# Kernel tuning notes

Hardware: AMD Instinct MI355X
Metric: run time of the kernel (lower is better)

## Reference

```python
import jax, jax.numpy as jnp
import numpy as np

B, T = 2, 512
D, H, DFF = 1024, 16, 4096
V, CSL = 32000, 16
NL, NDL = 4, 2
MAXLEN = 1024
DH = D // H


def generate_ar_mask(L, csl):
    m = np.zeros((2 * L, 2 * L), dtype=bool)
    for i in range(L):
        m[:i] = True
        m[L + (i // csl) * csl: L + i] = True
    return jnp.asarray(m)


def generate_block_ntp_mask(L, csl):
    m = np.zeros((2 * L, 2 * L), dtype=bool)
    for c in range(L // csl):
        if c - 1 >= 0:
            m[:(c - 1) * csl] = True
        m[L + c * csl: L + (c + 1) * csl] = True
    return jnp.asarray(m)


def layernorm(x, g, b, eps=1e-5):
    mu = x.mean(-1, keepdims=True)
    var = x.var(-1, keepdims=True)
    return (x - mu) / jnp.sqrt(var + eps) * g + b


def block(x, mask, p):
    ln1g, ln1b, wqkv, bqkv, wo, bo, ln2g, ln2b, w1, b1, w2, b2 = p
    h = layernorm(x, ln1g, ln1b)
    qkv = h @ wqkv + bqkv                       # [B,S,3D]
    q, k, v = jnp.split(qkv, 3, axis=-1)
    bs, S, _ = x.shape
    q = q.reshape(bs, S, H, DH).transpose(0, 2, 1, 3)
    k = k.reshape(bs, S, H, DH).transpose(0, 2, 1, 3)
    v = v.reshape(bs, S, H, DH).transpose(0, 2, 1, 3)
    scores = jnp.einsum('bhqd,bhkd->bhqk', q, k) / jnp.sqrt(jnp.asarray(DH, x.dtype))
    scores = jnp.where(mask, scores, jnp.asarray(-1e9, x.dtype))
    attn = jax.nn.softmax(scores, axis=-1)
    o = jnp.einsum('bhqk,bhkd->bhqd', attn, v)
    o = o.transpose(0, 2, 1, 3).reshape(bs, S, D)
    x = x + (o @ wo + bo)
    h = layernorm(x, ln2g, ln2b)
    return x + (jax.nn.gelu(h @ w1 + b1, approximate=False) @ w2 + b2)


def setup_inputs():
    key = jax.random.key(0)
    ks = jax.random.split(key, 6)

    def pstack(k, n):
        kk = jax.random.split(k, 4)
        return dict(
            ln1g=jnp.ones((n, D)), ln1b=jnp.zeros((n, D)),
            wqkv=0.02 * jax.random.normal(kk[0], (n, D, 3 * D)), bqkv=jnp.zeros((n, 3 * D)),
            wo=0.02 * jax.random.normal(kk[1], (n, D, D)), bo=jnp.zeros((n, D)),
            ln2g=jnp.ones((n, D)), ln2b=jnp.zeros((n, D)),
            w1=0.02 * jax.random.normal(kk[2], (n, D, DFF)), b1=jnp.zeros((n, DFF)),
            w2=0.02 * jax.random.normal(kk[3], (n, DFF, D)), b2=jnp.zeros((n, D)))

    body = pstack(ks[0], NL)
    dec = pstack(ks[1], NDL)
    inp = {
        'tok_ids': jax.random.randint(ks[2], (B, T), 0, V),
        'tok_emb': 0.02 * jax.random.normal(ks[3], (V, D)),
        'pos_emb': 0.02 * jax.random.normal(ks[4], (MAXLEN, D)),
        'mask_tokens': 0.02 * jax.random.normal(ks[5], (1, CSL, D)),
    }
    for kname, vv in body.items():
        inp['b_' + kname] = vv
    for kname, vv in dec.items():
        inp['d_' + kname] = vv
    return inp


def reference(tok_ids, tok_emb, pos_emb, mask_tokens,
              b_ln1g, b_ln1b, b_wqkv, b_bqkv, b_wo, b_bo, b_ln2g, b_ln2b, b_w1, b_b1, b_w2, b_b2,
              d_ln1g, d_ln1b, d_wqkv, d_bqkv, d_wo, d_bo, d_ln2g, d_ln2b, d_w1, d_b1, d_w2, d_b2):
    Bq, Tq = tok_ids.shape
    pos = jnp.tile(jnp.arange(Tq), 2)            # pos ids repeated for both halves
    emb_pos = pos_emb[pos]                       # [2T, D], broadcast over batch
    mask_ids = jnp.tile(mask_tokens, (Bq, Tq // CSL, 1))
    x = jnp.concatenate([tok_emb[tok_ids], mask_ids], axis=1) + emb_pos[None]

    body_mask = generate_block_ntp_mask(Tq, CSL)
    bp = (b_ln1g, b_ln1b, b_wqkv, b_bqkv, b_wo, b_bo, b_ln2g, b_ln2b, b_w1, b_b1, b_w2, b_b2)
    for i in range(NL):
        x = block(x, body_mask, tuple(p[i] for p in bp))

    ar_mask = generate_ar_mask(Tq, CSL)
    dp = (d_ln1g, d_ln1b, d_wqkv, d_bqkv, d_wo, d_bo, d_ln2g, d_ln2b, d_w1, d_b1, d_w2, d_b2)
    for i in range(NDL):
        x = block(x, ar_mask, tuple(p[i] for p in dp))

    logits = (x @ tok_emb.T)[:, Tq + 1:, :]      # [B, T-1, V]
    tgt = tok_ids[:, :-1].reshape(-1)
    logits = logits.reshape(-1, V)
    logp = jax.nn.log_softmax(logits, axis=-1)
    loss = -jnp.take_along_axis(logp, tgt[:, None], axis=1).mean()
    return loss
```

## Files before the change

kernel.cpp:

```cpp
#include <hip/hip_runtime.h>
#include <hip/hip_bf16.h>
#include <math.h>

#define DD   1024
#define HHN  16
#define DHD  64
#define DFFN 4096
#define VV   32000
#define BBN  2
#define TTN  512
#define SSN  1024
#define NRN  2048

typedef __attribute__((ext_vector_type(8))) short short8;
typedef __attribute__((ext_vector_type(4))) float f32x4;

enum : long {
    LSTR    = 12582912,
    OFF_QKV = 0,
    OFF_WO  = 3145728,
    OFF_W1  = 4194304,
    OFF_W2  = 8388608
};

struct P24 { const float* p[24]; };

__device__ __forceinline__ unsigned short f2bf(float f) {
    __hip_bfloat16 h = __float2bfloat16(f);
    return __builtin_bit_cast(unsigned short, h);
}
__device__ __forceinline__ float bf2f(unsigned short u) {
    return __bfloat162float(__builtin_bit_cast(__hip_bfloat16, u));
}

__device__ __forceinline__ void glds16(const void* g, void* l) {
    __builtin_amdgcn_global_load_lds(
        (const __attribute__((address_space(1))) void*)g,
        (__attribute__((address_space(3))) void*)l,
        16, 0, 0);
}

__device__ __forceinline__ float blockReduceSum(float v) {
    __shared__ float sh[4];
    #pragma unroll
    for (int o = 1; o < 64; o <<= 1) v += __shfl_xor(v, o, 64);
    int lane = threadIdx.x & 63, wv = threadIdx.x >> 6;
    __syncthreads();
    if (lane == 0) sh[wv] = v;
    __syncthreads();
    return sh[0] + sh[1] + sh[2] + sh[3];
}

__global__ __launch_bounds__(256) void prep_k(P24 wp, unsigned short* __restrict__ wbf,
                                              const int* __restrict__ tok,
                                              const float* __restrict__ temb,
                                              const float* __restrict__ pemb,
                                              const float* __restrict__ mtok,
                                              float* __restrict__ x) {
    __shared__ __align__(16) unsigned short Lb[256][72];
    const int id = blockIdx.x;
    const int t = threadIdx.x;

    if (id < 4608) {
        int seg, base, K, N;
        long woff;
        if (id < 1152)      { seg = 0; base = 0;    K = DD;   N = 3 * DD; woff = OFF_QKV; }
        else if (id < 1536) { seg = 1; base = 1152; K = DD;   N = DD;     woff = OFF_WO;  }
        else if (id < 3072) { seg = 2; base = 1536; K = DD;   N = DFFN;   woff = OFF_W1;  }
        else                { seg = 3; base = 3072; K = DFFN; N = DD;     woff = OFF_W2;  }
        const int rid = id - base;
        const int tpl = (K / 256) * (N / 64);
        const int lz = rid / tpl, t2 = rid % tpl;
        const int nt = N / 64;
        const int n0 = (t2 % nt) * 64, k0 = (t2 / nt) * 256;
        const float* w = wp.p[seg * 6 + lz];
        unsigned short* wt = wbf + (size_t)lz * LSTR + woff;

        #pragma unroll
        for (int p = 0; p < 2; p++) {
            const int k = p * 128 + (t >> 1);
            const int nch = (t & 1) * 32;
            const float* src = w + (size_t)(k0 + k) * N + n0 + nch;
            __align__(16) unsigned short tmp[32];
            #pragma unroll
            for (int i = 0; i < 8; i++) {
                float4 f = ((const float4*)src)[i];
                tmp[i * 4 + 0] = f2bf(f.x); tmp[i * 4 + 1] = f2bf(f.y);
                tmp[i * 4 + 2] = f2bf(f.z); tmp[i * 4 + 3] = f2bf(f.w);
            }
            #pragma unroll
            for (int i = 0; i < 4; i++)
                *(int4*)&Lb[k][nch + i * 8] = *(const int4*)&tmp[i * 8];
        }
        __syncthreads();
        {
            const int row = t >> 2, kc = (t & 3) * 64;
            __align__(16) unsigned short tmp[64];
            #pragma unroll
            for (int i = 0; i < 64; i++) tmp[i] = Lb[kc + i][row];
            unsigned short* dst = wt + (size_t)(n0 + row) * K + k0 + kc;
            #pragma unroll
            for (int i = 0; i < 8; i++)
                *(int4*)(dst + i * 8) = *(const int4*)&tmp[i * 8];
        }
    } else {
        const int row = id - 4608;
        const int b = row >> 10, s = row & 1023;
        const int d = t * 4;
        const float* src;
        const float* pe;
        if (s < TTN) {
            int tid2 = tok[b * TTN + s];
            src = temb + (size_t)tid2 * DD + d;
            pe  = pemb + (size_t)s * DD + d;
        } else {
            int sm = s - TTN;
            src = mtok + (size_t)(sm & 15) * DD + d;
            pe  = pemb + (size_t)sm * DD + d;
        }
        float4 v = *(const float4*)src;
        float4 p = *(const float4*)pe;
        v.x += p.x; v.y += p.y; v.z += p.z; v.w += p.w;
        *(float4*)(x + (size_t)row * DD + d) = v;
    }
}

__global__ __launch_bounds__(256) void ln_k(const float* __restrict__ x,
                                            const float* __restrict__ g,
                                            const float* __restrict__ b,
                                            unsigned short* __restrict__ out) {
    int row = blockIdx.x;
    int d = threadIdx.x * 4;
    const float4 v = *(const float4*)(x + (size_t)row * DD + d);
    float s  = v.x + v.y + v.z + v.w;
    float ss = v.x * v.x + v.y * v.y + v.z * v.z + v.w * v.w;
    s  = blockReduceSum(s);
    ss = blockReduceSum(ss);
    float mu  = s * (1.0f / DD);
    float var = ss * (1.0f / DD) - mu * mu;
    float inv = rsqrtf(var + 1e-5f);
    const float4 gg = *(const float4*)(g + d);
    const float4 bb = *(const float4*)(b + d);
    ushort4 o;
    o.x = f2bf((v.x - mu) * inv * gg.x + bb.x);
    o.y = f2bf((v.y - mu) * inv * gg.y + bb.y);
    o.z = f2bf((v.z - mu) * inv * gg.z + bb.z);
    o.w = f2bf((v.w - mu) * inv * gg.w + bb.w);
    *(ushort4*)(out + (size_t)row * DD + d) = o;
}

__global__ __launch_bounds__(256) void conv_k(const float* __restrict__ w,
                                              unsigned short* __restrict__ o, long n) {
    long i = ((long)blockIdx.x * 256 + threadIdx.x) * 8;
    if (i >= n) return;
    float4 a = *(const float4*)(w + i);
    float4 b = *(const float4*)(w + i + 4);
    __align__(16) unsigned short tmp[8];
    tmp[0] = f2bf(a.x); tmp[1] = f2bf(a.y); tmp[2] = f2bf(a.z); tmp[3] = f2bf(a.w);
    tmp[4] = f2bf(b.x); tmp[5] = f2bf(b.y); tmp[6] = f2bf(b.z); tmp[7] = f2bf(b.w);
    *(int4*)(o + i) = *(const int4*)tmp;
}

__global__ __launch_bounds__(256, 4) void flash_k(
    const unsigned short* __restrict__ qkvb,
    unsigned short* __restrict__ o,
    int mtype) {
    __shared__ __align__(16) unsigned short Qs[64][72];
    __shared__ __align__(16) unsigned short Ks[64][72];
    __shared__ __align__(16) unsigned short Vs[64][72];
    __shared__ __align__(16) unsigned short Ps[64][72];
    __shared__ float vcol[64];

    const int blk = blockIdx.x;
    const int bh = blk >> 4, qt = blk & 15;
    const int b = bh >> 4, h = bh & 15;
    const int t = threadIdx.x;
    const int lane = t & 63;
    const int w = t >> 6;
    const int fr = lane & 15;
    const int g8 = (lane >> 4) * 8;
    const int g4 = (lane >> 4) * 4;

    {
        const int r = t >> 2, c0 = (t & 3) * 16;
        const unsigned short* src =
            qkvb + (size_t)(b * SSN + qt * 64 + r) * 3072 + h * 64 + c0;
        *(int4*)&Qs[r][c0]     = *(const int4*)(src);
        *(int4*)&Qs[r][c0 + 8] = *(const int4*)(src + 8);
    }
    __syncthreads();
    short8 aq[2];
    #pragma unroll
    for (int kk = 0; kk < 2; kk++)
        aq[kk] = *(const short8*)&Qs[w * 16 + fr][kk * 32 + g8];

    float mrun[4], lrun[4];
    f32x4 accO[4] = {};
    #pragma unroll
    for (int j = 0; j < 4; j++) { mrun[j] = -1e30f; lrun[j] = 0.f; }

    float vacc[16];
    #pragma unroll
    for (int j = 0; j < 16; j++) vacc[j] = 0.f;

    const unsigned short* kbase = qkvb + (size_t)(b * SSN) * 3072 + DD + h * 64;
    const unsigned short* vbase = qkvb + (size_t)(b * SSN) * 3072 + 2 * DD + h * 64;
    const int d0 = w * 16;

    for (int kt = 0; kt < 16; kt++) {
        __syncthreads();
        {
            const int r = t >> 2, c0 = (t & 3) * 16;
            const unsigned short* src = kbase + (size_t)(kt * 64 + r) * 3072 + c0;
            *(int4*)&Ks[r][c0]     = *(const int4*)(src);
            *(int4*)&Ks[r][c0 + 8] = *(const int4*)(src + 8);
        }
        {
            const unsigned short* src = vbase + (size_t)(kt * 64 + lane) * 3072 + d0;
            int4 q0 = *(const int4*)(src);
            int4 q1 = *(const int4*)(src + 8);
            const unsigned short* u = (const unsigned short*)&q0;
            #pragma unroll
            for (int j = 0; j < 8; j++) {
                Vs[d0 + j][lane] = u[j];
                vacc[j] += bf2f(u[j]);
            }
            const unsigned short* u2 = (const unsigned short*)&q1;
            #pragma unroll
            for (int j = 0; j < 8; j++) {
                Vs[d0 + 8 + j][lane] = u2[j];
                vacc[8 + j] += bf2f(u2[j]);
            }
        }
        __syncthreads();

        f32x4 a2[4] = {};
        #pragma unroll
        for (int n = 0; n < 4; n++) {
            short8 bk0 = *(const short8*)&Ks[n * 16 + fr][g8];
            short8 bk1 = *(const short8*)&Ks[n * 16 + fr][32 + g8];
            a2[n] = __builtin_amdgcn_mfma_f32_16x16x32_bf16(aq[0], bk0, a2[n], 0, 0, 0);
            a2[n] = __builtin_amdgcn_mfma_f32_16x16x32_bf16(aq[1], bk1, a2[n], 0, 0, 0);
        }
        #pragma unroll
        for (int j = 0; j < 4; j++) {
            float tm = fmaxf(fmaxf(a2[0][j], a2[1][j]), fmaxf(a2[2][j], a2[3][j]));
            tm *= 0.125f;
            #pragma unroll
            for (int o2 = 1; o2 < 16; o2 <<= 1) tm = fmaxf(tm, __shfl_xor(tm, o2, 64));
            const float mn = fmaxf(mrun[j], tm);
            const float alpha = __expf(mrun[j] - mn);
            mrun[j] = mn;
            float rs = 0.f;
            #pragma unroll
            for (int n = 0; n < 4; n++) {
                float pv = __expf(a2[n][j] * 0.125f - mn);
                rs += pv;
                Ps[w * 16 + g4 + j][n * 16 + fr] = f2bf(pv);
            }
            #pragma unroll
            for (int o2 = 1; o2 < 16; o2 <<= 1) rs += __shfl_xor(rs, o2, 64);
            lrun[j] = lrun[j] * alpha + rs;
            #pragma unroll
            for (int nd = 0; nd < 4; nd++) accO[nd][j] *= alpha;
        }
        #pragma unroll
        for (int kk = 0; kk < 2; kk++) {
            short8 pa = *(const short8*)&Ps[w * 16 + fr][kk * 32 + g8];
            #pragma unroll
            for (int nd = 0; nd < 4; nd++) {
                short8 vb = *(const short8*)&Vs[nd * 16 + fr][kk * 32 + g8];
                accO[nd] = __builtin_amdgcn_mfma_f32_16x16x32_bf16(pa, vb, accO[nd], 0, 0, 0);
            }
        }
    }

    #pragma unroll
    for (int j = 0; j < 16; j++) {
        float vs = vacc[j];
        #pragma unroll
        for (int o2 = 1; o2 < 64; o2 <<= 1) vs += __shfl_xor(vs, o2, 64);
        if (lane == j) vcol[d0 + j] = vs;
    }
    __syncthreads();

    #pragma unroll
    for (int nd = 0; nd < 4; nd++)
        #pragma unroll
        for (int j = 0; j < 4; j++) {
            const int row = qt * 64 + w * 16 + g4 + j;
            const int col = nd * 16 + fr;
            bool uni;
            if (mtype == 0) uni = (row >= 480 && row < 512);
            else            uni = (row == 511) || (row >= 512 && (row & 15) == 15);
            float val;
            if (uni) val = vcol[col] * (1.0f / 1024.0f);
            else     val = accO[nd][j] / lrun[j];
            o[(size_t)(b * SSN + row) * DD + h * 64 + col] = f2bf(val);
        }
}

template <bool DOLN>
__global__ __launch_bounds__(256) void rln_k(const float* __restrict__ pp,
                                             const float* __restrict__ bias,
                                             float* __restrict__ x,
                                             const float* __restrict__ g,
                                             const float* __restrict__ b,
                                             unsigned short* __restrict__ xb,
                                             unsigned short* __restrict__ xl) {
    const int row = blockIdx.x;
    const int d = threadIdx.x * 4;
    const size_t off = (size_t)row * DD + d;
    float4 v = *(const float4*)(x + off);
    #pragma unroll
    for (int sl = 0; sl < 4; sl++) {
        float4 p = *(const float4*)(pp + (size_t)sl * NRN * DD + off);
        v.x += p.x; v.y += p.y; v.z += p.z; v.w += p.w;
    }
    const float4 bv = *(const float4*)(bias + d);
    v.x += bv.x; v.y += bv.y; v.z += bv.z; v.w += bv.w;
    *(float4*)(x + off) = v;
    if (DOLN) {
        float s  = v.x + v.y + v.z + v.w;
        float ss = v.x * v.x + v.y * v.y + v.z * v.z + v.w * v.w;
        s  = blockReduceSum(s);
        ss = blockReduceSum(ss);
        float mu  = s * (1.0f / DD);
        float var = ss * (1.0f / DD) - mu * mu;
        float inv = rsqrtf(var + 1e-5f);
        const float4 gg = *(const float4*)(g + d);
        const float4 bb = *(const float4*)(b + d);
        ushort4 ov;
        ov.x = f2bf((v.x - mu) * inv * gg.x + bb.x);
        ov.y = f2bf((v.y - mu) * inv * gg.y + bb.y);
        ov.z = f2bf((v.z - mu) * inv * gg.z + bb.z);
        ov.w = f2bf((v.w - mu) * inv * gg.w + bb.w);
        *(ushort4*)(xb + off) = ov;
    } else {
        const int s = row & 1023;
        if (s >= 513) {
            const int xr = (row >> 10) * 511 + (s - 513);
            ushort4 ov;
            ov.x = f2bf(v.x); ov.y = f2bf(v.y); ov.z = f2bf(v.z); ov.w = f2bf(v.w);
            *(ushort4*)(xl + (size_t)xr * DD + d) = ov;
        }
    }
}

__global__ __launch_bounds__(256) void loss_row2_k(const float2* __restrict__ part,
                                                   const float* __restrict__ tgtlog,
                                                   float* __restrict__ rowloss) {
    const int r = blockIdx.x;
    const int t = threadIdx.x;
    float mx = -1e30f, s = 0.f;
    for (int i = t; i < 500; i += 256) {
        float2 p = part[(size_t)r * 500 + i];
        float m2 = fmaxf(mx, p.x);
        s = s * __expf(mx - m2) + p.y * __expf(p.x - m2);
        mx = m2;
    }
    #pragma unroll
    for (int o2 = 1; o2 < 64; o2 <<= 1) {
        float om = __shfl_xor(mx, o2, 64);
        float os = __shfl_xor(s, o2, 64);
        float m2 = fmaxf(mx, om);
        s = s * __expf(mx - m2) + os * __expf(om - m2);
        mx = m2;
    }
    __shared__ float shm[4], shs[4];
    int lane = t & 63, wv = t >> 6;
    if (lane == 0) { shm[wv] = mx; shs[wv] = s; }
    __syncthreads();
    if (t == 0) {
        float M = fmaxf(fmaxf(shm[0], shm[1]), fmaxf(shm[2], shm[3]));
        float S = shs[0] * __expf(shm[0] - M) + shs[1] * __expf(shm[1] - M)
                + shs[2] * __expf(shm[2] - M) + shs[3] * __expf(shm[3] - M);
        rowloss[r] = (logf(S) + M) - tgtlog[r];
    }
}

__global__ __launch_bounds__(256) void loss_final_k(const float* __restrict__ rowloss,
                                                    float* __restrict__ out) {
    int t = threadIdx.x;
    float s = 0.f;
    for (int i = t; i < 1022; i += 256) s += rowloss[i];
    s = blockReduceSum(s);
    if (t == 0) out[0] = s * (1.0f / 1022.0f);
}

template <int EPI, int KSPLIT>
__global__ __launch_bounds__(256) void gemm_k(
    const unsigned short* __restrict__ A, long lda,
    const unsigned short* __restrict__ Bt, long ldb,
    void* __restrict__ Cp, long ldc,
    const float* __restrict__ bias,
    int MT, int K, long kstr) {
    __shared__ __align__(16) unsigned short As[2][128][32];
    __shared__ __align__(16) unsigned short Bs[2][128][32];

    const int nwg = gridDim.x;
    const int q = nwg >> 3, r = nwg & 7;
    const int xcd = blockIdx.x & 7, lin = blockIdx.x >> 3;
    const int wg = (xcd < r ? xcd * (q + 1) : r * (q + 1) + (xcd - r) * q) + lin;
    const int tiles = nwg / KSPLIT;
    const int ks = wg / tiles;
    const int rem = wg % tiles;
    const int brow = (rem % MT) * 128;
    const int bcol = (rem / MT) * 128;
    const int Kl = K / KSPLIT;

    const int t = threadIdx.x;
    const int lane = t & 63;
    const int w = t >> 6;
    const int fr = lane & 15;
    const int g8 = (lane >> 4) * 8;

    const int sr = w * 32 + (lane >> 2);
    const int sc = (lane & 3) * 8;
    const unsigned short* aP0 = A + (size_t)(brow + sr) * lda + ks * Kl + sc;
    const unsigned short* aP1 = aP0 + (size_t)16 * lda;
    const unsigned short* bP0 = Bt + (size_t)(bcol + sr) * ldb + ks * Kl + sc;
    const unsigned short* bP1 = bP0 + (size_t)16 * ldb;

    f32x4 acc[4][4] = {};
    const int nsteps = Kl >> 5;

    glds16(aP0, &As[0][w * 32][0]);
    glds16(aP1, &As[0][w * 32 + 16][0]);
    glds16(bP0, &Bs[0][w * 32][0]);
    glds16(bP1, &Bs[0][w * 32 + 16][0]);
    aP0 += 32; aP1 += 32; bP0 += 32; bP1 += 32;
    asm volatile("s_waitcnt vmcnt(0)");
    __syncthreads();

    int cur = 0;
    for (int s2 = 1; s2 < nsteps; ++s2) {
        const int nb = cur ^ 1;
        glds16(aP0, &As[nb][w * 32][0]);
        glds16(aP1, &As[nb][w * 32 + 16][0]);
        glds16(bP0, &Bs[nb][w * 32][0]);
        glds16(bP1, &Bs[nb][w * 32 + 16][0]);
        aP0 += 32; aP1 += 32; bP0 += 32; bP1 += 32;

        short8 af[4], bf[4];
        #pragma unroll
        for (int m = 0; m < 4; m++)
            af[m] = *(const short8*)&As[cur][(w >> 1) * 64 + m * 16 + fr][g8];
        #pragma unroll
        for (int n = 0; n < 4; n++)
            bf[n] = *(const short8*)&Bs[cur][(w & 1) * 64 + n * 16 + fr][g8];
        #pragma unroll
        for (int m = 0; m < 4; m++)
            #pragma unroll
            for (int n = 0; n < 4; n++)
                acc[m][n] = __builtin_amdgcn_mfma_f32_16x16x32_bf16(af[m], bf[n], acc[m][n], 0, 0, 0);
        __syncthreads();
        cur = nb;
    }
    {
        short8 af[4], bf[4];
        #pragma unroll
        for (int m = 0; m < 4; m++)
            af[m] = *(const short8*)&As[cur][(w >> 1) * 64 + m * 16 + fr][g8];
        #pragma unroll
        for (int n = 0; n < 4; n++)
            bf[n] = *(const short8*)&Bs[cur][(w & 1) * 64 + n * 16 + fr][g8];
        #pragma unroll
        for (int m = 0; m < 4; m++)
            #pragma unroll
            for (int n = 0; n < 4; n++)
                acc[m][n] = __builtin_amdgcn_mfma_f32_16x16x32_bf16(af[m], bf[n], acc[m][n], 0, 0, 0);
    }

    const int wr = (w >> 1) * 64;
    const int wc = (w & 1) * 64;
    const int g4 = (lane >> 4) * 4;
    #pragma unroll
    for (int n = 0; n < 4; n++) {
        const int col = bcol + wc + n * 16 + fr;
        const float bv = bias ? bias[col] : 0.f;
        #pragma unroll
        for (int m = 0; m < 4; m++) {
            #pragma unroll
            for (int j = 0; j < 4; j++) {
                const int row = brow + wr + m * 16 + g4 + j;
                float v = acc[m][n][j] + bv;
                const size_t ci = (size_t)row * ldc + col;
                if (EPI == 0) {
                    ((float*)Cp)[ci] = v;
                } else if (EPI == 1) {
                    ((unsigned short*)Cp)[ci] = f2bf(v);
                } else if (EPI == 2) {
                    float gl = 0.5f * v * (1.0f + erff(v * 0.70710678118654752f));
                    ((unsigned short*)Cp)[ci] = f2bf(gl);
                } else if (EPI == 3) {
                    ((float*)Cp)[ci] += v;
                } else {
                    ((float*)Cp)[(size_t)ks * kstr + ci] = v;
                }
            }
        }
    }
}

__global__ __launch_bounds__(256) void gemm_lse_k(
    const unsigned short* __restrict__ A,
    const unsigned short* __restrict__ Bt,
    float2* __restrict__ part,
    float* __restrict__ tgtlog,
    const int* __restrict__ tok) {
    __shared__ __align__(16) unsigned short As[2][128][32];
    __shared__ __align__(16) unsigned short Bs[2][128][32];

    const int nwg = gridDim.x;
    const int q = nwg >> 3, r = nwg & 7;
    const int xcd = blockIdx.x & 7, lin = blockIdx.x >> 3;
    const int wg = (xcd < r ? xcd * (q + 1) : r * (q + 1) + (xcd - r) * q) + lin;
    const int MT = 8;
    const int brow = (wg % MT) * 128;
    const int bcol = (wg / MT) * 128;

    const int t = threadIdx.x;
    const int lane = t & 63;
    const int w = t >> 6;
    const int fr = lane & 15;
    const int g8 = (lane >> 4) * 8;

    const int sr = w * 32 + (lane >> 2);
    const int sc = (lane & 3) * 8;
    const unsigned short* aP0 = A + (size_t)(brow + sr) * DD + sc;
    const unsigned short* aP1 = aP0 + (size_t)16 * DD;
    const unsigned short* bP0 = Bt + (size_t)(bcol + sr) * DD + sc;
    const unsigned short* bP1 = bP0 + (size_t)16 * DD;

    f32x4 acc[4][4] = {};

    glds16(aP0, &As[0][w * 32][0]);
    glds16(aP1, &As[0][w * 32 + 16][0]);
    glds16(bP0, &Bs[0][w * 32][0]);
    glds16(bP1, &Bs[0][w * 32 + 16][0]);
    aP0 += 32; aP1 += 32; bP0 += 32; bP1 += 32;
    asm volatile("s_waitcnt vmcnt(0)");
    __syncthreads();

    int cur = 0;
    for (int s2 = 1; s2 < 32; ++s2) {
        const int nb = cur ^ 1;
        glds16(aP0, &As[nb][w * 32][0]);
        glds16(aP1, &As[nb][w * 32 + 16][0]);
        glds16(bP0, &Bs[nb][w * 32][0]);
        glds16(bP1, &Bs[nb][w * 32 + 16][0]);
        aP0 += 32; aP1 += 32; bP0 += 32; bP1 += 32;

        short8 af[4], bf[4];
        #pragma unroll
        for (int m = 0; m < 4; m++)
            af[m] = *(const short8*)&As[cur][(w >> 1) * 64 + m * 16 + fr][g8];
        #pragma unroll
        for (int n = 0; n < 4; n++)
            bf[n] = *(const short8*)&Bs[cur][(w & 1) * 64 + n * 16 + fr][g8];
        #pragma unroll
        for (int m = 0; m < 4; m++)
            #pragma unroll
            for (int n = 0; n < 4; n++)
                acc[m][n] = __builtin_amdgcn_mfma_f32_16x16x32_bf16(af[m], bf[n], acc[m][n], 0, 0, 0);
        __syncthreads();
        cur = nb;
    }
    {
        short8 af[4], bf[4];
        #pragma unroll
        for (int m = 0; m < 4; m++)
            af[m] = *(const short8*)&As[cur][(w >> 1) * 64 + m * 16 + fr][g8];
        #pragma unroll
        for (int n = 0; n < 4; n++)
            bf[n] = *(const short8*)&Bs[cur][(w & 1) * 64 + n * 16 + fr][g8];
        #pragma unroll
        for (int m = 0; m < 4; m++)
            #pragma unroll
            for (int n = 0; n < 4; n++)
                acc[m][n] = __builtin_amdgcn_mfma_f32_16x16x32_bf16(af[m], bf[n], acc[m][n], 0, 0, 0);
    }

    const int wr = (w >> 1) * 64;
    const int wc = (w & 1) * 64;
    const int g4 = (lane >> 4) * 4;
    const int ct2 = (bcol >> 7) * 2 + (w & 1);
    #pragma unroll
    for (int m = 0; m < 4; m++) {
        #pragma unroll
        for (int j = 0; j < 4; j++) {
            const int grow = brow + wr + m * 16 + g4 + j;
            const float v0 = acc[m][0][j], v1 = acc[m][1][j];
            const float v2 = acc[m][2][j], v3 = acc[m][3][j];
            float mx = fmaxf(fmaxf(v0, v1), fmaxf(v2, v3));
            #pragma unroll
            for (int o2 = 1; o2 < 16; o2 <<= 1) mx = fmaxf(mx, __shfl_xor(mx, o2, 64));
            float s = __expf(v0 - mx) + __expf(v1 - mx) + __expf(v2 - mx) + __expf(v3 - mx);
            #pragma unroll
            for (int o2 = 1; o2 < 16; o2 <<= 1) s += __shfl_xor(s, o2, 64);
            if (fr == 0) {
                float2 p; p.x = mx; p.y = s;
                part[(size_t)grow * 500 + ct2] = p;
            }
            int tgtc = -1;
            if (grow < 511) tgtc = tok[grow];
            else if (grow >= 511 && grow < 1022) tgtc = tok[512 + grow - 511];
            const int cl = tgtc - (bcol + wc);
            if (tgtc >= 0 && cl >= 0 && cl < 64 && (cl & 15) == fr) {
                const float vv[4] = {v0, v1, v2, v3};
                tgtlog[grow] = vv[cl >> 4];
            }
        }
    }
}

extern "C" void kernel_launch(void* const* d_in, const int* in_sizes, int n_in,
                              void* d_out, int out_size, void* d_ws, size_t ws_size,
                              hipStream_t stream) {
    const int*   tok  = (const int*)d_in[0];
    const float* temb = (const float*)d_in[1];
    const float* pemb = (const float*)d_in[2];
    const float* mtok = (const float*)d_in[3];
    const float* W[24];
    for (int i = 0; i < 24; i++) W[i] = (const float*)d_in[4 + i];

    char* ws = (char*)d_ws;
    float*          x      = (float*)(ws + 0);
    unsigned short* xb     = (unsigned short*)(ws + 8388608);
    unsigned short* qkvb   = (unsigned short*)(ws + 12582912);
    unsigned short* o      = (unsigned short*)(ws + 25165824);
    unsigned short* g      = (unsigned short*)(ws + 29360128);
    float*          pp     = (float*)(ws + 46137344);
    unsigned short* wbf    = (unsigned short*)(ws + 79691776);
    unsigned short* tembb  = (unsigned short*)(ws + 79691776);
    float2*         part   = (float2*)(ws + 145227776);
    float*          tgtlog = (float*)(ws + 149327872);
    unsigned short* xl     = (unsigned short*)(ws + 230686720);
    float*          rowloss= (float*)(ws + 232783872);

    P24 wp;
    for (int l = 0; l < 6; l++) {
        const int grp = (l < 4) ? 0 : 1;
        const int li  = (l < 4) ? l : l - 4;
        const float* const* P = W + grp * 12;
        wp.p[0 + l]  = P[2]  + (size_t)li * DD * 3 * DD;
        wp.p[6 + l]  = P[4]  + (size_t)li * DD * DD;
        wp.p[12 + l] = P[8]  + (size_t)li * DD * DFFN;
        wp.p[18 + l] = P[10] + (size_t)li * DFFN * DD;
    }
    prep_k<<<4608 + 2048, 256, 0, stream>>>(wp, wbf, tok, temb, pemb, mtok, x);

    for (int l = 0; l < 6; l++) {
        const int grp = (l < 4) ? 0 : 1;
        const int li  = (l < 4) ? l : l - 4;
        const float* const* P = W + grp * 12;
        const float* ln1g = P[0] + (size_t)li * DD;
        const float* ln1b = P[1] + (size_t)li * DD;
        const float* bqkv = P[3] + (size_t)li * 3 * DD;
        const float* bo   = P[5] + (size_t)li * DD;
        const float* ln2g = P[6] + (size_t)li * DD;
        const float* ln2b = P[7] + (size_t)li * DD;
        const float* b1   = P[9] + (size_t)li * DFFN;
        const float* b2   = P[11] + (size_t)li * DD;
        unsigned short* wl = wbf + (size_t)l * LSTR;

        if (l == 0) ln_k<<<NRN, 256, 0, stream>>>(x, ln1g, ln1b, xb);
        gemm_k<1, 1><<<16 * 24, 256, 0, stream>>>(xb, DD, wl + OFF_QKV, DD,
                                                  qkvb, 3 * DD, bqkv, 16, DD, 0);
        flash_k<<<512, 256, 0, stream>>>(qkvb, o, grp);
        gemm_k<3, 1><<<16 * 8, 256, 0, stream>>>(o, DD, wl + OFF_WO, DD,
                                                 x, DD, bo, 16, DD, 0);

        ln_k<<<NRN, 256, 0, stream>>>(x, ln2g, ln2b, xb);
        gemm_k<2, 1><<<16 * 32, 256, 0, stream>>>(xb, DD, wl + OFF_W1, DD,
                                                  g, DFFN, b1, 16, DD, 0);
        gemm_k<4, 4><<<16 * 8 * 4, 256, 0, stream>>>(g, DFFN, wl + OFF_W2, DFFN,
                                                     pp, DD, nullptr, 16, DFFN,
                                                     (long)NRN * DD);
        if (l < 5) {
            const int l2 = l + 1;
            const int grp2 = (l2 < 4) ? 0 : 1;
            const int li2  = (l2 < 4) ? l2 : l2 - 4;
            const float* const* P2 = W + grp2 * 12;
            rln_k<true><<<NRN, 256, 0, stream>>>(pp, b2, x,
                                                 P2[0] + (size_t)li2 * DD,
                                                 P2[1] + (size_t)li2 * DD, xb, nullptr);
        } else {
            rln_k<false><<<NRN, 256, 0, stream>>>(pp, b2, x, nullptr, nullptr, nullptr, xl);
        }
    }

    conv_k<<<16000, 256, 0, stream>>>(temb, tembb, (long)VV * DD);
    gemm_lse_k<<<2000, 256, 0, stream>>>(xl, tembb, part, tgtlog, tok);
    loss_row2_k<<<1022, 256, 0, stream>>>(part, tgtlog, rowloss);
    loss_final_k<<<1, 256, 0, stream>>>(rowloss, (float*)d_out);
}
```

Measured before the change: 1.554 ms.

## Add 64-row GEMM tiles for QKV/WO and swizzle weight-transpose LDS

Templates the GEMM on the M tile height and uses 64-row tiles for the QKV and output-projection GEMMs, doubling their workgroup counts (768 and 256) so more of the GPU's CUs get work. It also rewrites the weight-conversion transpose in prep_k to use XOR-swizzled LDS addressing and 32-bit paired reads, cutting bank conflicts and scalar LDS reads. Smaller tiles lower per-block data reuse and MFMA density, trading some arithmetic efficiency for parallelism.

```diff
diff --git a/kernel.cpp b/kernel.cpp
--- a/kernel.cpp
+++ b/kernel.cpp
@@ -57,7 +57,7 @@
                                               const float* __restrict__ pemb,
                                               const float* __restrict__ mtok,
                                               float* __restrict__ x) {
-    __shared__ __align__(16) unsigned short Lb[256][72];
+    __shared__ __align__(16) unsigned short Lb[256 * 72];
     const int id = blockIdx.x;
     const int t = threadIdx.x;
 
@@ -80,6 +80,7 @@
         for (int p = 0; p < 2; p++) {
             const int k = p * 128 + (t >> 1);
             const int nch = (t & 1) * 32;
+            const int g = ((k >> 6) & 3) << 4;
             const float* src = w + (size_t)(k0 + k) * N + n0 + nch;
             __align__(16) unsigned short tmp[32];
             #pragma unroll
@@ -90,18 +91,29 @@
             }
             #pragma unroll
             for (int i = 0; i < 4; i++)
-                *(int4*)&Lb[k][nch + i * 8] = *(const int4*)&tmp[i * 8];
+                *(int4*)&Lb[k * 72 + ((nch + i * 8) ^ g)] = *(const int4*)&tmp[i * 8];
         }
         __syncthreads();
         {
-            const int row = t >> 2, kc = (t & 3) * 64;
-            __align__(16) unsigned short tmp[64];
-            #pragma unroll
-            for (int i = 0; i < 64; i++) tmp[i] = Lb[kc + i][row];
-            unsigned short* dst = wt + (size_t)(n0 + row) * K + k0 + kc;
-            #pragma unroll
-            for (int i = 0; i < 8; i++)
-                *(int4*)(dst + i * 8) = *(const int4*)&tmp[i * 8];
+            const int rp  = t >> 3;
+            const int sub = t & 7;
+            const int kcg = sub & 3, kh = sub >> 2;
+            const int colx = (2 * rp) ^ (kcg << 4);
+            const int kb = kcg * 64 + kh * 32;
+            __align__(16) unsigned short tA[32], tB[32];
+            #pragma unroll
+            for (int i = 0; i < 32; i++) {
+                unsigned int v = *(const unsigned int*)&Lb[(kb + i) * 72 + colx];
+                tA[i] = (unsigned short)(v & 0xffff);
+                tB[i] = (unsigned short)(v >> 16);
+            }
+            unsigned short* d0 = wt + (size_t)(n0 + 2 * rp) * K + k0 + kb;
+            unsigned short* d1 = d0 + K;
+            #pragma unroll
+            for (int i = 0; i < 4; i++) {
+                ((int4*)d0)[i] = ((const int4*)tA)[i];
+                ((int4*)d1)[i] = ((const int4*)tB)[i];
+            }
         }
     } else {
         const int row = id - 4608;
@@ -388,14 +400,15 @@
     if (t == 0) out[0] = s * (1.0f / 1022.0f);
 }
 
-template <int EPI, int KSPLIT>
+template <int EPI, int KSPLIT, int BM>
 __global__ __launch_bounds__(256) void gemm_k(
     const unsigned short* __restrict__ A, long lda,
     const unsigned short* __restrict__ Bt, long ldb,
     void* __restrict__ Cp, long ldc,
     const float* __restrict__ bias,
     int MT, int K, long kstr) {
-    __shared__ __align__(16) unsigned short As[2][128][32];
+    constexpr int MFRAG = BM / 32;
+    __shared__ __align__(16) unsigned short As[2][BM][32];
     __shared__ __align__(16) unsigned short Bs[2][128][32];
 
     const int nwg = gridDim.x;
@@ -405,7 +418,7 @@
     const int tiles = nwg / KSPLIT;
     const int ks = wg / tiles;
     const int rem = wg % tiles;
-    const int brow = (rem % MT) * 128;
+    const int brow = (rem % MT) * BM;
     const int bcol = (rem / MT) * 128;
     const int Kl = K / KSPLIT;
 
@@ -415,42 +428,48 @@
     const int fr = lane & 15;
     const int g8 = (lane >> 4) * 8;
 
-    const int sr = w * 32 + (lane >> 2);
     const int sc = (lane & 3) * 8;
-    const unsigned short* aP0 = A + (size_t)(brow + sr) * lda + ks * Kl + sc;
+    const int srB = w * 32 + (lane >> 2);
+    const unsigned short* bP0 = Bt + (size_t)(bcol + srB) * ldb + ks * Kl + sc;
+    const unsigned short* bP1 = bP0 + (size_t)16 * ldb;
+    const int srA = (BM == 128 ? w * 32 : w * 16) + (lane >> 2);
+    const unsigned short* aP0 = A + (size_t)(brow + srA) * lda + ks * Kl + sc;
     const unsigned short* aP1 = aP0 + (size_t)16 * lda;
-    const unsigned short* bP0 = Bt + (size_t)(bcol + sr) * ldb + ks * Kl + sc;
-    const unsigned short* bP1 = bP0 + (size_t)16 * ldb;
-
-    f32x4 acc[4][4] = {};
+
+    f32x4 acc[MFRAG][4] = {};
     const int nsteps = Kl >> 5;
 
-    glds16(aP0, &As[0][w * 32][0]);
-    glds16(aP1, &As[0][w * 32 + 16][0]);
-    glds16(bP0, &Bs[0][w * 32][0]);
-    glds16(bP1, &Bs[0][w * 32 + 16][0]);
-    aP0 += 32; aP1 += 32; bP0 += 32; bP1 += 32;
+    auto stage = [&](int buf) {
+        if constexpr (BM == 128) {
+            glds16(aP0, &As[buf][w * 32][0]);
+            glds16(aP1, &As[buf][w * 32 + 16][0]);
+        } else {
+            glds16(aP0, &As[buf][w * 16][0]);
+        }
+        glds16(bP0, &Bs[buf][w * 32][0]);
+        glds16(bP1, &Bs[buf][w * 32 + 16][0]);
+        aP0 += 32; aP1 += 32; bP0 += 32; bP1 += 32;
+    };
+
+    stage(0);
     asm volatile("s_waitcnt vmcnt(0)");
     __syncthreads();
 
+    const int wrB = (w >> 1) * (BM / 2);
     int cur = 0;
     for (int s2 = 1; s2 < nsteps; ++s2) {
         const int nb = cur ^ 1;
-        glds16(aP0, &As[nb][w * 32][0]);
-        glds16(aP1, &As[nb][w * 32 + 16][0]);
-        glds16(bP0, &Bs[nb][w * 32][0]);
-        glds16(bP1, &Bs[nb][w * 32 + 16][0]);
-        aP0 += 32; aP1 += 32; bP0 += 32; bP1 += 32;
-
-        short8 af[4], bf[4];
-        #pragma unroll
-        for (int m = 0; m < 4; m++)
-            af[m] = *(const short8*)&As[cur][(w >> 1) * 64 + m * 16 + fr][g8];
+        stage(nb);
+
+        short8 af[MFRAG], bf[4];
+        #pragma unroll
+        for (int m = 0; m < MFRAG; m++)
+            af[m] = *(const short8*)&As[cur][wrB + m * 16 + fr][g8];
         #pragma unroll
         for (int n = 0; n < 4; n++)
             bf[n] = *(const short8*)&Bs[cur][(w & 1) * 64 + n * 16 + fr][g8];
         #pragma unroll
-        for (int m = 0; m < 4; m++)
+        for (int m = 0; m < MFRAG; m++)
             #pragma unroll
             for (int n = 0; n < 4; n++)
                 acc[m][n] = __builtin_amdgcn_mfma_f32_16x16x32_bf16(af[m], bf[n], acc[m][n], 0, 0, 0);
@@ -458,21 +477,20 @@
         cur = nb;
     }
     {
-        short8 af[4], bf[4];
-        #pragma unroll
-        for (int m = 0; m < 4; m++)
-            af[m] = *(const short8*)&As[cur][(w >> 1) * 64 + m * 16 + fr][g8];
+        short8 af[MFRAG], bf[4];
+        #pragma unroll
+        for (int m = 0; m < MFRAG; m++)
+            af[m] = *(const short8*)&As[cur][wrB + m * 16 + fr][g8];
         #pragma unroll
         for (int n = 0; n < 4; n++)
             bf[n] = *(const short8*)&Bs[cur][(w & 1) * 64 + n * 16 + fr][g8];
         #pragma unroll
-        for (int m = 0; m < 4; m++)
+        for (int m = 0; m < MFRAG; m++)
             #pragma unroll
             for (int n = 0; n < 4; n++)
                 acc[m][n] = __builtin_amdgcn_mfma_f32_16x16x32_bf16(af[m], bf[n], acc[m][n], 0, 0, 0);
     }
 
-    const int wr = (w >> 1) * 64;
     const int wc = (w & 1) * 64;
     const int g4 = (lane >> 4) * 4;
     #pragma unroll
@@ -480,10 +498,10 @@
         const int col = bcol + wc + n * 16 + fr;
         const float bv = bias ? bias[col] : 0.f;
         #pragma unroll
-        for (int m = 0; m < 4; m++) {
+        for (int m = 0; m < MFRAG; m++) {
             #pragma unroll
             for (int j = 0; j < 4; j++) {
-                const int row = brow + wr + m * 16 + g4 + j;
+                const int row = brow + wrB + m * 16 + g4 + j;
                 float v = acc[m][n][j] + bv;
                 const size_t ci = (size_t)row * ldc + col;
                 if (EPI == 0) {
@@ -666,18 +684,18 @@
         unsigned short* wl = wbf + (size_t)l * LSTR;
 
         if (l == 0) ln_k<<<NRN, 256, 0, stream>>>(x, ln1g, ln1b, xb);
-        gemm_k<1, 1><<<16 * 24, 256, 0, stream>>>(xb, DD, wl + OFF_QKV, DD,
-                                                  qkvb, 3 * DD, bqkv, 16, DD, 0);
+        gemm_k<1, 1, 64><<<32 * 24, 256, 0, stream>>>(xb, DD, wl + OFF_QKV, DD,
+                                                      qkvb, 3 * DD, bqkv, 32, DD, 0);
         flash_k<<<512, 256, 0, stream>>>(qkvb, o, grp);
-        gemm_k<3, 1><<<16 * 8, 256, 0, stream>>>(o, DD, wl + OFF_WO, DD,
-                                                 x, DD, bo, 16, DD, 0);
+        gemm_k<3, 1, 64><<<32 * 8, 256, 0, stream>>>(o, DD, wl + OFF_WO, DD,
+                                                     x, DD, bo, 32, DD, 0);
 
         ln_k<<<NRN, 256, 0, stream>>>(x, ln2g, ln2b, xb);
-        gemm_k<2, 1><<<16 * 32, 256, 0, stream>>>(xb, DD, wl + OFF_W1, DD,
-                                                  g, DFFN, b1, 16, DD, 0);
-        gemm_k<4, 4><<<16 * 8 * 4, 256, 0, stream>>>(g, DFFN, wl + OFF_W2, DFFN,
-                                                     pp, DD, nullptr, 16, DFFN,
-                                                     (long)NRN * DD);
+        gemm_k<2, 1, 128><<<16 * 32, 256, 0, stream>>>(xb, DD, wl + OFF_W1, DD,
+                                                       g, DFFN, b1, 16, DD, 0);
+        gemm_k<4, 4, 128><<<16 * 8 * 4, 256, 0, stream>>>(g, DFFN, wl + OFF_W2, DFFN,
+                                                          pp, DD, nullptr, 16, DFFN,
+                                                          (long)NRN * DD);
         if (l < 5) {
             const int l2 = l + 1;
             const int grp2 = (l2 < 4) ? 0 : 1;
```

Result: faster. 1.495 ms (-3.8%).
